# Optimization experiments

Hardware: AMD Instinct MI355X
Metric: run time of the kernel (lower is better)

The kernel has to match this reference:

```python
import jax, jax.numpy as jnp
import numpy as np

N_NODES = 100000
N_EDGES = 3200000
F_IN = 512
HIDDEN = 16
N_CLASSES = 64
EPS = 1e-12  # F.normalize eps


def agnn_layer(x, src, dst, beta, n_nodes):
    """AGNNConv: cosine-similarity attention + segment softmax + scatter aggregate.
    x: [N, H]; src/dst: [E] (messages flow src -> dst, softmax over edges per dst).
    """
    norm = jnp.sqrt(jnp.sum(x * x, axis=-1, keepdims=True))
    xn = x / jnp.maximum(norm, EPS)                      # L2-normalized features
    cos = jnp.sum(xn[src] * xn[dst], axis=-1)            # [E] cosine similarity
    logits = beta * cos
    m = jax.ops.segment_max(logits, dst, num_segments=n_nodes)   # stable softmax per dst
    e = jnp.exp(logits - m[dst])
    denom = jax.ops.segment_sum(e, dst, num_segments=n_nodes)
    alpha = e / denom[dst]                               # [E]
    return jax.ops.segment_sum(alpha[:, None] * x[src], dst, num_segments=n_nodes)


def setup_inputs() -> dict:
    key = jax.random.key(0)
    ks = jax.random.split(key, 6)
    x = jax.random.normal(ks[0], (N_NODES, F_IN), dtype=jnp.float32)
    edge_index = jax.random.randint(ks[1], (2, N_EDGES), 0, N_NODES, dtype=jnp.int64)
    W1 = jax.random.normal(ks[2], (F_IN, HIDDEN), dtype=jnp.float32) * (1.0 / np.sqrt(F_IN))
    b1 = jnp.zeros((HIDDEN,), dtype=jnp.float32)
    W2 = jax.random.normal(ks[3], (HIDDEN, N_CLASSES), dtype=jnp.float32) * (1.0 / np.sqrt(HIDDEN))
    b2 = jnp.zeros((N_CLASSES,), dtype=jnp.float32)
    beta1 = jnp.ones((), dtype=jnp.float32)  # AGNNConv beta init = 1.0
    beta2 = jnp.ones((), dtype=jnp.float32)
    return {"x": x, "edge_index": edge_index, "W1": W1, "b1": b1,
            "W2": W2, "b2": b2, "beta1": beta1, "beta2": beta2}


def reference(x, edge_index, W1, b1, W2, b2, beta1, beta2):
    n = x.shape[0]
    # PyG AGNNConv adds self-loops before propagation
    loops = jnp.arange(n, dtype=edge_index.dtype)
    src = jnp.concatenate([edge_index[0], loops])
    dst = jnp.concatenate([edge_index[1], loops])
    # eval mode: dropout is identity
    h = jax.nn.relu(x @ W1 + b1)                 # [N, 16]
    h = agnn_layer(h, src, dst, beta1, n)
    h = agnn_layer(h, src, dst, beta2, n)
    out = h @ W2 + b2                            # [N, num_classes]
    return jax.nn.log_softmax(out, axis=1)
```

## Files before the change

### kernel.cpp

```cpp
#include <hip/hip_runtime.h>
#include <hip/hip_bf16.h>

#define F_IN 512
#define HID 16
#define NCLS 64
#define NBUCK_MAX 512
#define EPB 8192

__device__ __forceinline__ void gemm_rows(
    const float* __restrict__ x, const float* __restrict__ W1,
    const float* __restrict__ b1, float* __restrict__ h0,
    float* __restrict__ inv0, int rB, int rE, int wid, int totalWaves, int lane)
{
    float bias = b1[lane & 15];
    const bool s3 = (lane & 8) != 0;
    const bool s2 = (lane & 4) != 0;
    const bool s1 = (lane & 2) != 0;
    const bool s0 = (lane & 1) != 0;

    for (int g = rB + wid * 4; g < rE; g += totalWaves * 4) {
        int r0 = g;
        int r1 = (g + 1 < rE) ? g + 1 : rE - 1;
        int r2 = (g + 2 < rE) ? g + 2 : rE - 1;
        int r3 = (g + 3 < rE) ? g + 3 : rE - 1;

        float xv[4][8];
        {
            const float4* xp0 = (const float4*)(x + (size_t)r0 * F_IN + 8 * lane);
            const float4* xp1 = (const float4*)(x + (size_t)r1 * F_IN + 8 * lane);
            const float4* xp2 = (const float4*)(x + (size_t)r2 * F_IN + 8 * lane);
            const float4* xp3 = (const float4*)(x + (size_t)r3 * F_IN + 8 * lane);
            float4 a, b;
            a = xp0[0]; b = xp0[1];
            xv[0][0]=a.x; xv[0][1]=a.y; xv[0][2]=a.z; xv[0][3]=a.w;
            xv[0][4]=b.x; xv[0][5]=b.y; xv[0][6]=b.z; xv[0][7]=b.w;
            a = xp1[0]; b = xp1[1];
            xv[1][0]=a.x; xv[1][1]=a.y; xv[1][2]=a.z; xv[1][3]=a.w;
            xv[1][4]=b.x; xv[1][5]=b.y; xv[1][6]=b.z; xv[1][7]=b.w;
            a = xp2[0]; b = xp2[1];
            xv[2][0]=a.x; xv[2][1]=a.y; xv[2][2]=a.z; xv[2][3]=a.w;
            xv[2][4]=b.x; xv[2][5]=b.y; xv[2][6]=b.z; xv[2][7]=b.w;
            a = xp3[0]; b = xp3[1];
            xv[3][0]=a.x; xv[3][1]=a.y; xv[3][2]=a.z; xv[3][3]=a.w;
            xv[3][4]=b.x; xv[3][5]=b.y; xv[3][6]=b.z; xv[3][7]=b.w;
        }

        float acc[4][16];
#pragma unroll
        for (int i = 0; i < 4; ++i)
#pragma unroll
            for (int j = 0; j < 16; ++j) acc[i][j] = 0.f;

#pragma unroll
        for (int kk = 0; kk < 8; ++kk) {
            const float4* wp = (const float4*)(W1 + (size_t)(8 * lane + kk) * HID);
#pragma unroll
            for (int jj = 0; jj < 4; ++jj) {
                float4 t = wp[jj];
#pragma unroll
                for (int i = 0; i < 4; ++i) {
                    float xs = xv[i][kk];
                    acc[i][jj * 4 + 0] += xs * t.x;
                    acc[i][jj * 4 + 1] += xs * t.y;
                    acc[i][jj * 4 + 2] += xs * t.z;
                    acc[i][jj * 4 + 3] += xs * t.w;
                }
            }
        }

        int rr[4] = {r0, r1, r2, r3};
#pragma unroll
        for (int i = 0; i < 4; ++i) {
            float* a = acc[i];
#pragma unroll
            for (int u = 0; u < 8; ++u) {
                float k = s3 ? a[u + 8] : a[u];
                float s = s3 ? a[u] : a[u + 8];
                a[u] = k + __shfl_xor(s, 8);
            }
#pragma unroll
            for (int u = 0; u < 4; ++u) {
                float k = s2 ? a[u + 4] : a[u];
                float s = s2 ? a[u] : a[u + 4];
                a[u] = k + __shfl_xor(s, 4);
            }
#pragma unroll
            for (int u = 0; u < 2; ++u) {
                float k = s1 ? a[u + 2] : a[u];
                float s = s1 ? a[u] : a[u + 2];
                a[u] = k + __shfl_xor(s, 2);
            }
            {
                float k = s0 ? a[1] : a[0];
                float s = s0 ? a[0] : a[1];
                a[0] = k + __shfl_xor(s, 1);
            }
            a[0] += __shfl_xor(a[0], 16);
            a[0] += __shfl_xor(a[0], 32);

            float val = fmaxf(a[0] + bias, 0.f);
            bool live = (g + i < rE);
            if (live && lane < 16) h0[(size_t)rr[i] * HID + lane] = val;

            float qq = val * val;
            qq += __shfl_xor(qq, 1);
            qq += __shfl_xor(qq, 2);
            qq += __shfl_xor(qq, 4);
            qq += __shfl_xor(qq, 8);
            if (live && lane == 0) inv0[rr[i]] = 1.f / fmaxf(sqrtf(qq), 1e-12f);
        }
    }
}

__global__ __launch_bounds__(256) void hist1_kernel(
    const int* __restrict__ dst, int E, int EV, int nbuck,
    int* __restrict__ bucketCount)
{
    __shared__ int h[NBUCK_MAX];
    int tid = threadIdx.x;
    for (int j = tid; j < nbuck; j += 256) h[j] = 0;
    __syncthreads();
    int base = blockIdx.x * EPB;
    for (int k = 0; k < EPB / 256; ++k) {
        int i = base + k * 256 + tid;
        if (i < EV) {
            int d = (i < E) ? dst[i] : (i - E);
            atomicAdd(&h[d >> 8], 1);
        }
    }
    __syncthreads();
    for (int j = tid; j < nbuck; j += 256)
        if (h[j]) atomicAdd(&bucketCount[j], h[j]);
}

__global__ __launch_bounds__(512) void bucket_scan_kernel(
    const int* __restrict__ bucketCount, int nbuck,
    int* __restrict__ bucketStart, int* __restrict__ gCursor)
{
    __shared__ int s[512];
    int t = threadIdx.x;
    int v = (t < nbuck) ? bucketCount[t] : 0;
    s[t] = v;
    __syncthreads();
    for (int off = 1; off < 512; off <<= 1) {
        int add = (t >= off) ? s[t - off] : 0;
        __syncthreads();
        s[t] += add;
        __syncthreads();
    }
    int incl = s[t];
    if (t < nbuck) {
        bucketStart[t] = incl - v;
        gCursor[t]     = incl - v;
        if (t == nbuck - 1) bucketStart[nbuck] = incl;
    }
}

__global__ __launch_bounds__(256) void part_gemm_kernel(
    const int* __restrict__ src, const int* __restrict__ dst,
    int E, int EV, int nbuck, int* __restrict__ gCursor,
    unsigned* __restrict__ staged,
    const float* __restrict__ x, const float* __restrict__ W1,
    const float* __restrict__ b1, float* __restrict__ h0,
    float* __restrict__ inv0, int rB, int rE, int csrBlocks, int gemmWaves)
{
    __shared__ int h[NBUCK_MAX];
    __shared__ int gb[NBUCK_MAX];
    int tid = threadIdx.x;

    if ((int)blockIdx.x >= csrBlocks) {
        int wid = (((int)blockIdx.x - csrBlocks) * 256 + tid) >> 6;
        gemm_rows(x, W1, b1, h0, inv0, rB, rE, wid, gemmWaves, tid & 63);
        return;
    }

    for (int j = tid; j < nbuck; j += 256) h[j] = 0;
    __syncthreads();

    int base = blockIdx.x * EPB;
    for (int k = 0; k < EPB / 256; ++k) {
        int i = base + k * 256 + tid;
        if (i < EV) {
            int d = (i < E) ? dst[i] : (i - E);
            atomicAdd(&h[d >> 8], 1);
        }
    }
    __syncthreads();
    for (int j = tid; j < nbuck; j += 256) {
        int c = h[j];
        if (c) gb[j] = atomicAdd(&gCursor[j], c);
        h[j] = 0;
    }
    __syncthreads();
    for (int k = 0; k < EPB / 256; ++k) {
        int i = base + k * 256 + tid;
        if (i < EV) {
            int s, d;
            if (i < E) { s = src[i]; d = dst[i]; }
            else       { s = i - E;  d = s; }
            int bkt = d >> 8;
            int ofs = atomicAdd(&h[bkt], 1);
            staged[gb[bkt] + ofs] = (unsigned)s | ((unsigned)(d & 255) << 17);
        }
    }
}

__global__ __launch_bounds__(256) void build_gemm_kernel(
    const unsigned* __restrict__ staged, const int* __restrict__ bucketStart,
    int* __restrict__ counts, int* __restrict__ rowstart,
    int* __restrict__ esrc, int N,
    const float* __restrict__ x, const float* __restrict__ W1,
    const float* __restrict__ b1, float* __restrict__ h0,
    float* __restrict__ inv0, int rB, int rE, int csrBlocks, int gemmWaves)
{
    __shared__ int hist[256];
    __shared__ int s[256];
    __shared__ int cur[256];
    int tid = threadIdx.x;

    if ((int)blockIdx.x >= csrBlocks) {
        int wid = (((int)blockIdx.x - csrBlocks) * 256 + tid) >> 6;
        gemm_rows(x, W1, b1, h0, inv0, rB, rE, wid, gemmWaves, tid & 63);
        return;
    }

    int b   = blockIdx.x;
    int start = bucketStart[b];
    int end   = bucketStart[b + 1];

    hist[tid] = 0;
    __syncthreads();
    for (int i = start + tid; i < end; i += 256)
        atomicAdd(&hist[(staged[i] >> 17) & 255], 1);
    __syncthreads();

    int v = hist[tid];
    s[tid] = v;
    __syncthreads();
    for (int off = 1; off < 256; off <<= 1) {
        int add = (tid >= off) ? s[tid - off] : 0;
        __syncthreads();
        s[tid] += add;
        __syncthreads();
    }
    int excl = s[tid] - v;
    int dstg = b * 256 + tid;
    if (dstg < N) {
        counts[dstg]   = v;
        rowstart[dstg] = start + excl;
    }
    cur[tid] = start + excl;
    __syncthreads();

    for (int i = start + tid; i < end; i += 256) {
        unsigned pk = staged[i];
        int dl  = (pk >> 17) & 255;
        int pos = atomicAdd(&cur[dl], 1);
        esrc[pos] = (int)(pk & 0x1FFFFu);
    }
}

__global__ __launch_bounds__(256) void agg_kernel(
    const float* __restrict__ h, const float* __restrict__ inv,
    const int* __restrict__ esrc, const int* __restrict__ rowstart,
    const int* __restrict__ counts, const float* __restrict__ beta_p,
    float* __restrict__ hout, float* __restrict__ invout, int N)
{
    int node = (blockIdx.x * blockDim.x + threadIdx.x) >> 6;
    if (node >= N) return;
    int lane = threadIdx.x & 63;
    int q = lane & 3;
    int e = lane >> 2;

    float beta  = *beta_p;
    float shift = fabsf(beta);
    float4 hd4  = ((const float4*)(h + (size_t)node * HID))[q];
    float  invd = inv[node];
    int start = rowstart[node];
    int cnt   = counts[node];

    int t0 = e, t1 = e + 16, t2 = e + 32, t3 = e + 48;
    int s0 = esrc[start + (t0 < cnt ? t0 : 0)];
    int s1 = esrc[start + (t1 < cnt ? t1 : 0)];
    int s2 = esrc[start + (t2 < cnt ? t2 : 0)];
    int s3 = esrc[start + (t3 < cnt ? t3 : 0)];
    const float4* hp = (const float4*)h;
    float4 a0 = hp[(size_t)s0 * 4 + q];
    float4 a1 = hp[(size_t)s1 * 4 + q];
    float4 a2 = hp[(size_t)s2 * 4 + q];
    float4 a3 = hp[(size_t)s3 * 4 + q];
    float i0 = inv[s0], i1 = inv[s1], i2 = inv[s2], i3 = inv[s3];

    float denom = 0.f;
    float4 acc = make_float4(0.f, 0.f, 0.f, 0.f);

#define AGG_SLOT(aa, ii, tt)                                                  \
    {                                                                         \
        float p = aa.x * hd4.x + aa.y * hd4.y + aa.z * hd4.z + aa.w * hd4.w;  \
        p += __shfl_xor(p, 1);                                                \
        p += __shfl_xor(p, 2);                                                \
        float w = __expf(beta * (p * invd * ii) - shift);                     \
        w = (tt < cnt) ? w : 0.f;                                             \
        denom += w;                                                           \
        acc.x += w * aa.x; acc.y += w * aa.y;                                 \
        acc.z += w * aa.z; acc.w += w * aa.w;                                 \
    }
    AGG_SLOT(a0, i0, t0)
    AGG_SLOT(a1, i1, t1)
    AGG_SLOT(a2, i2, t2)
    AGG_SLOT(a3, i3, t3)
#undef AGG_SLOT

    for (int t = e + 64; t < cnt; t += 16) {
        int sr = esrc[start + t];
        float4 hs4 = hp[(size_t)sr * 4 + q];
        float invs = inv[sr];
        float p = hs4.x * hd4.x + hs4.y * hd4.y + hs4.z * hd4.z + hs4.w * hd4.w;
        p += __shfl_xor(p, 1);
        p += __shfl_xor(p, 2);
        float w = __expf(beta * (p * invd * invs) - shift);
        denom += w;
        acc.x += w * hs4.x;
        acc.y += w * hs4.y;
        acc.z += w * hs4.z;
        acc.w += w * hs4.w;
    }

#pragma unroll
    for (int off = 4; off <= 32; off <<= 1) {
        denom += __shfl_xor(denom, off);
        acc.x += __shfl_xor(acc.x, off);
        acc.y += __shfl_xor(acc.y, off);
        acc.z += __shfl_xor(acc.z, off);
        acc.w += __shfl_xor(acc.w, off);
    }
    float rd = 1.f / denom;
    float4 o = make_float4(acc.x * rd, acc.y * rd, acc.z * rd, acc.w * rd);
    if (lane < 4) ((float4*)(hout + (size_t)node * HID))[q] = o;

    float ss = o.x * o.x + o.y * o.y + o.z * o.z + o.w * o.w;
    ss += __shfl_xor(ss, 1);
    ss += __shfl_xor(ss, 2);
    if (lane == 0) invout[node] = 1.f / fmaxf(sqrtf(ss), 1e-12f);
}

__global__ __launch_bounds__(256) void out_kernel(
    const float* __restrict__ h2, const float* __restrict__ W2,
    const float* __restrict__ b2, float* __restrict__ out, int N)
{
    int wave = (blockIdx.x * blockDim.x + threadIdx.x) >> 6;
    int lane = threadIdx.x & 63;
    if (wave >= N) return;

    float hv = (lane < HID) ? h2[(size_t)wave * HID + lane] : 0.f;
    float acc = b2[lane];
#pragma unroll
    for (int k = 0; k < HID; ++k) {
        float hk = __shfl(hv, k);
        acc += hk * W2[k * NCLS + lane];
    }
    float m = acc;
    for (int off = 32; off > 0; off >>= 1) m = fmaxf(m, __shfl_xor(m, off));
    float e = __expf(acc - m);
    float ssum = e;
    for (int off = 32; off > 0; off >>= 1) ssum += __shfl_xor(ssum, off);
    out[(size_t)wave * NCLS + lane] = (acc - m) - __logf(ssum);
}

extern "C" void kernel_launch(void* const* d_in, const int* in_sizes, int n_in,
                              void* d_out, int out_size, void* d_ws, size_t ws_size,
                              hipStream_t stream)
{
    const float* x     = (const float*)d_in[0];
    const int*   eidx  = (const int*)d_in[1];
    const float* W1    = (const float*)d_in[2];
    const float* b1    = (const float*)d_in[3];
    const float* W2    = (const float*)d_in[4];
    const float* b2    = (const float*)d_in[5];
    const float* beta1 = (const float*)d_in[6];
    const float* beta2 = (const float*)d_in[7];

    int N = in_sizes[0] / F_IN;
    int E = in_sizes[1] / 2;
    const int* src = eidx;
    const int* dst = eidx + E;
    float* out = (float*)d_out;

    int EV    = E + N;
    int nbuck = (N + 255) / 256;

    char* wptr = (char*)d_ws;
    auto alloc = [&](size_t bytes) -> char* {
        char* p = wptr;
        wptr += (bytes + 255) / 256 * 256;
        return p;
    };
    float*    h0       = (float*)alloc((size_t)N * HID * 4);
    float*    inv0     = (float*)alloc((size_t)N * 4);
    float*    h1       = (float*)alloc((size_t)N * HID * 4);
    float*    inv1     = (float*)alloc((size_t)N * 4);
    float*    h2       = (float*)alloc((size_t)N * HID * 4);
    float*    inv2     = (float*)alloc((size_t)N * 4);
    int*      counts   = (int*)alloc((size_t)N * 4);
    int*      rowstart = (int*)alloc((size_t)(N + 1) * 4);
    int*      esrc     = (int*)alloc((size_t)EV * 4);
    unsigned* staged   = (unsigned*)alloc((size_t)EV * 4);
    int*      bucketCount = (int*)alloc((size_t)(nbuck + 1) * 4);
    int*      bucketStart = (int*)alloc((size_t)(nbuck + 1) * 4);
    int*      gCursor     = (int*)alloc((size_t)nbuck * 4);

    int ebBlocks = (EV + EPB - 1) / EPB;

    hipMemsetAsync(bucketCount, 0, (size_t)nbuck * 4, stream);
    hist1_kernel<<<ebBlocks, 256, 0, stream>>>(dst, E, EV, nbuck, bucketCount);
    bucket_scan_kernel<<<1, 512, 0, stream>>>(bucketCount, nbuck, bucketStart, gCursor);

    int rSplit   = 60000;
    int gcBlocks = 1024;
    int gdBlocks = 768;
    part_gemm_kernel<<<ebBlocks + gcBlocks, 256, 0, stream>>>(
        src, dst, E, EV, nbuck, gCursor, staged,
        x, W1, b1, h0, inv0, 0, rSplit, ebBlocks, gcBlocks * 4);
    build_gemm_kernel<<<nbuck + gdBlocks, 256, 0, stream>>>(
        staged, bucketStart, counts, rowstart, esrc, N,
        x, W1, b1, h0, inv0, rSplit, N, nbuck, gdBlocks * 4);

    int aggBlocks = (N + 3) / 4;
    agg_kernel<<<aggBlocks, 256, 0, stream>>>(h0, inv0, esrc, rowstart, counts, beta1,
                                              h1, inv1, N);
    agg_kernel<<<aggBlocks, 256, 0, stream>>>(h1, inv1, esrc, rowstart, counts, beta2,
                                              h2, inv2, N);

    out_kernel<<<(N * 64 + 255) / 256, 256, 0, stream>>>(h2, W2, b2, out, N);
}
```

Before: 552.5 us.

## Fuse partition, CSR build, GEMM, aggregations and output into one cooperative kernel

Replaces five separate launches (partition+GEMM, build+GEMM, two aggregation passes, output) with one persistent cooperative mega-kernel that uses grid.sync between phases. The partition and CSR build run on a quarter of the resident blocks while the rest compute the input GEMM. The GEMM inner loop drops from 4 rows to 2 rows per wave to cut register pressure for the occupancy hint. The aim is to remove launch gaps and kernel tails. The cost is grid-wide barriers, a grid capped by occupancy with grid-stride loops, and a fixed 55/45 GEMM split that may not balance the two phases.

```diff
diff --git a/kernel.cpp b/kernel.cpp
--- a/kernel.cpp
+++ b/kernel.cpp
@@ -1,5 +1,7 @@
 #include <hip/hip_runtime.h>
-#include <hip/hip_bf16.h>
+#include <hip/hip_cooperative_groups.h>
+
+namespace cg = cooperative_groups;
 
 #define F_IN 512
 #define HID 16
@@ -7,7 +9,7 @@
 #define NBUCK_MAX 512
 #define EPB 8192
 
-__device__ __forceinline__ void gemm_rows(
+__device__ __forceinline__ void gemm_rows2(
     const float* __restrict__ x, const float* __restrict__ W1,
     const float* __restrict__ b1, float* __restrict__ h0,
     float* __restrict__ inv0, int rB, int rE, int wid, int totalWaves, int lane)
@@ -18,18 +20,14 @@
     const bool s1 = (lane & 2) != 0;
     const bool s0 = (lane & 1) != 0;
 
-    for (int g = rB + wid * 4; g < rE; g += totalWaves * 4) {
+    for (int g = rB + wid * 2; g < rE; g += totalWaves * 2) {
         int r0 = g;
         int r1 = (g + 1 < rE) ? g + 1 : rE - 1;
-        int r2 = (g + 2 < rE) ? g + 2 : rE - 1;
-        int r3 = (g + 3 < rE) ? g + 3 : rE - 1;
-
-        float xv[4][8];
+
+        float xv[2][8];
         {
             const float4* xp0 = (const float4*)(x + (size_t)r0 * F_IN + 8 * lane);
             const float4* xp1 = (const float4*)(x + (size_t)r1 * F_IN + 8 * lane);
-            const float4* xp2 = (const float4*)(x + (size_t)r2 * F_IN + 8 * lane);
-            const float4* xp3 = (const float4*)(x + (size_t)r3 * F_IN + 8 * lane);
             float4 a, b;
             a = xp0[0]; b = xp0[1];
             xv[0][0]=a.x; xv[0][1]=a.y; xv[0][2]=a.z; xv[0][3]=a.w;
@@ -37,17 +35,11 @@
             a = xp1[0]; b = xp1[1];
             xv[1][0]=a.x; xv[1][1]=a.y; xv[1][2]=a.z; xv[1][3]=a.w;
             xv[1][4]=b.x; xv[1][5]=b.y; xv[1][6]=b.z; xv[1][7]=b.w;
-            a = xp2[0]; b = xp2[1];
-            xv[2][0]=a.x; xv[2][1]=a.y; xv[2][2]=a.z; xv[2][3]=a.w;
-            xv[2][4]=b.x; xv[2][5]=b.y; xv[2][6]=b.z; xv[2][7]=b.w;
-            a = xp3[0]; b = xp3[1];
-            xv[3][0]=a.x; xv[3][1]=a.y; xv[3][2]=a.z; xv[3][3]=a.w;
-            xv[3][4]=b.x; xv[3][5]=b.y; xv[3][6]=b.z; xv[3][7]=b.w;
-        }
-
-        float acc[4][16];
-#pragma unroll
-        for (int i = 0; i < 4; ++i)
+        }
+
+        float acc[2][16];
+#pragma unroll
+        for (int i = 0; i < 2; ++i)
 #pragma unroll
             for (int j = 0; j < 16; ++j) acc[i][j] = 0.f;
 
@@ -58,7 +50,7 @@
             for (int jj = 0; jj < 4; ++jj) {
                 float4 t = wp[jj];
 #pragma unroll
-                for (int i = 0; i < 4; ++i) {
+                for (int i = 0; i < 2; ++i) {
                     float xs = xv[i][kk];
                     acc[i][jj * 4 + 0] += xs * t.x;
                     acc[i][jj * 4 + 1] += xs * t.y;
@@ -68,9 +60,9 @@
             }
         }
 
-        int rr[4] = {r0, r1, r2, r3};
-#pragma unroll
-        for (int i = 0; i < 4; ++i) {
+        int rr[2] = {r0, r1};
+#pragma unroll
+        for (int i = 0; i < 2; ++i) {
             float* a = acc[i];
 #pragma unroll
             for (int u = 0; u < 8; ++u) {
@@ -109,6 +101,118 @@
             qq += __shfl_xor(qq, 8);
             if (live && lane == 0) inv0[rr[i]] = 1.f / fmaxf(sqrtf(qq), 1e-12f);
         }
+    }
+}
+
+__device__ __forceinline__ void agg_phase(
+    const float* __restrict__ h, const float* __restrict__ inv,
+    const int* __restrict__ esrc, const int* __restrict__ rowstart,
+    const int* __restrict__ counts, const float* __restrict__ beta_p,
+    float* __restrict__ hout, float* __restrict__ invout, int N, int G)
+{
+    int w = blockIdx.x * 4 + (threadIdx.x >> 6);
+    int W = G * 4;
+    int lane = threadIdx.x & 63;
+    int q = lane & 3;
+    int e = lane >> 2;
+
+    float beta  = *beta_p;
+    float shift = fabsf(beta);
+    const float4* hp = (const float4*)h;
+
+    for (int node = w; node < N; node += W) {
+        float4 hd4  = hp[(size_t)node * 4 + q];
+        float  invd = inv[node];
+        int start = rowstart[node];
+        int cnt   = counts[node];
+
+        int t0 = e, t1 = e + 16, t2 = e + 32, t3 = e + 48;
+        int s0 = esrc[start + (t0 < cnt ? t0 : 0)];
+        int s1 = esrc[start + (t1 < cnt ? t1 : 0)];
+        int s2 = esrc[start + (t2 < cnt ? t2 : 0)];
+        int s3 = esrc[start + (t3 < cnt ? t3 : 0)];
+        float4 a0 = hp[(size_t)s0 * 4 + q];
+        float4 a1 = hp[(size_t)s1 * 4 + q];
+        float4 a2 = hp[(size_t)s2 * 4 + q];
+        float4 a3 = hp[(size_t)s3 * 4 + q];
+        float i0 = inv[s0], i1 = inv[s1], i2 = inv[s2], i3 = inv[s3];
+
+        float denom = 0.f;
+        float4 acc = make_float4(0.f, 0.f, 0.f, 0.f);
+
+#define AGG_SLOT(aa, ii, tt)                                                  \
+        {                                                                     \
+            float p = aa.x*hd4.x + aa.y*hd4.y + aa.z*hd4.z + aa.w*hd4.w;      \
+            p += __shfl_xor(p, 1);                                            \
+            p += __shfl_xor(p, 2);                                            \
+            float wgt = __expf(beta * (p * invd * ii) - shift);               \
+            wgt = (tt < cnt) ? wgt : 0.f;                                     \
+            denom += wgt;                                                     \
+            acc.x += wgt * aa.x; acc.y += wgt * aa.y;                         \
+            acc.z += wgt * aa.z; acc.w += wgt * aa.w;                         \
+        }
+        AGG_SLOT(a0, i0, t0)
+        AGG_SLOT(a1, i1, t1)
+        AGG_SLOT(a2, i2, t2)
+        AGG_SLOT(a3, i3, t3)
+#undef AGG_SLOT
+
+        for (int t = e + 64; t < cnt; t += 16) {
+            int sr = esrc[start + t];
+            float4 hs4 = hp[(size_t)sr * 4 + q];
+            float invs = inv[sr];
+            float p = hs4.x*hd4.x + hs4.y*hd4.y + hs4.z*hd4.z + hs4.w*hd4.w;
+            p += __shfl_xor(p, 1);
+            p += __shfl_xor(p, 2);
+            float wgt = __expf(beta * (p * invd * invs) - shift);
+            denom += wgt;
+            acc.x += wgt * hs4.x;
+            acc.y += wgt * hs4.y;
+            acc.z += wgt * hs4.z;
+            acc.w += wgt * hs4.w;
+        }
+
+#pragma unroll
+        for (int off = 4; off <= 32; off <<= 1) {
+            denom += __shfl_xor(denom, off);
+            acc.x += __shfl_xor(acc.x, off);
+            acc.y += __shfl_xor(acc.y, off);
+            acc.z += __shfl_xor(acc.z, off);
+            acc.w += __shfl_xor(acc.w, off);
+        }
+        float rd = 1.f / denom;
+        float4 o = make_float4(acc.x * rd, acc.y * rd, acc.z * rd, acc.w * rd);
+        if (lane < 4) ((float4*)(hout + (size_t)node * HID))[q] = o;
+
+        float ss = o.x*o.x + o.y*o.y + o.z*o.z + o.w*o.w;
+        ss += __shfl_xor(ss, 1);
+        ss += __shfl_xor(ss, 2);
+        if (lane == 0) invout[node] = 1.f / fmaxf(sqrtf(ss), 1e-12f);
+    }
+}
+
+__device__ __forceinline__ void out_phase(
+    const float* __restrict__ h2, const float* __restrict__ W2,
+    const float* __restrict__ b2, float* __restrict__ out, int N, int G)
+{
+    int w = blockIdx.x * 4 + (threadIdx.x >> 6);
+    int W = G * 4;
+    int lane = threadIdx.x & 63;
+
+    for (int row = w; row < N; row += W) {
+        float hv = (lane < HID) ? h2[(size_t)row * HID + lane] : 0.f;
+        float acc = b2[lane];
+#pragma unroll
+        for (int k = 0; k < HID; ++k) {
+            float hk = __shfl(hv, k);
+            acc += hk * W2[k * NCLS + lane];
+        }
+        float m = acc;
+        for (int off = 32; off > 0; off >>= 1) m = fmaxf(m, __shfl_xor(m, off));
+        float e = __expf(acc - m);
+        float ssum = e;
+        for (int off = 32; off > 0; off >>= 1) ssum += __shfl_xor(ssum, off);
+        out[(size_t)row * NCLS + lane] = (acc - m) - __logf(ssum);
     }
 }
 
@@ -156,215 +260,114 @@
     }
 }
 
-__global__ __launch_bounds__(256) void part_gemm_kernel(
-    const int* __restrict__ src, const int* __restrict__ dst,
-    int E, int EV, int nbuck, int* __restrict__ gCursor,
-    unsigned* __restrict__ staged,
-    const float* __restrict__ x, const float* __restrict__ W1,
-    const float* __restrict__ b1, float* __restrict__ h0,
-    float* __restrict__ inv0, int rB, int rE, int csrBlocks, int gemmWaves)
-{
-    __shared__ int h[NBUCK_MAX];
-    __shared__ int gb[NBUCK_MAX];
+struct MegaArgs {
+    const int* src; const int* dst; int E; int EV; int nbuck;
+    int* gCursor; unsigned* staged;
+    const int* bucketStart; int* counts; int* rowstart; int* esrc; int N;
+    const float* x; const float* W1; const float* b1;
+    float* h0; float* inv0; float* h1; float* inv1; float* h2; float* inv2;
+    const float* beta1; const float* beta2;
+    const float* W2; const float* b2; float* out;
+    int C; int G; int splitA;
+};
+
+__global__ __launch_bounds__(256, 6) void mega_kernel(MegaArgs a)
+{
+    cg::grid_group grid = cg::this_grid();
+    __shared__ int lh[NBUCK_MAX];
+    __shared__ int lg[NBUCK_MAX];
+    int bid = blockIdx.x;
     int tid = threadIdx.x;
-
-    if ((int)blockIdx.x >= csrBlocks) {
-        int wid = (((int)blockIdx.x - csrBlocks) * 256 + tid) >> 6;
-        gemm_rows(x, W1, b1, h0, inv0, rB, rE, wid, gemmWaves, tid & 63);
-        return;
-    }
-
-    for (int j = tid; j < nbuck; j += 256) h[j] = 0;
-    __syncthreads();
-
-    int base = blockIdx.x * EPB;
-    for (int k = 0; k < EPB / 256; ++k) {
-        int i = base + k * 256 + tid;
-        if (i < EV) {
-            int d = (i < E) ? dst[i] : (i - E);
-            atomicAdd(&h[d >> 8], 1);
-        }
-    }
-    __syncthreads();
-    for (int j = tid; j < nbuck; j += 256) {
-        int c = h[j];
-        if (c) gb[j] = atomicAdd(&gCursor[j], c);
-        h[j] = 0;
-    }
-    __syncthreads();
-    for (int k = 0; k < EPB / 256; ++k) {
-        int i = base + k * 256 + tid;
-        if (i < EV) {
+    int lane = tid & 63;
+
+    if (bid < a.C) {
+        int chunk = (a.EV + a.C - 1) / a.C;
+        int base = bid * chunk;
+        int lim  = base + chunk; if (lim > a.EV) lim = a.EV;
+
+        for (int j = tid; j < a.nbuck; j += 256) lh[j] = 0;
+        __syncthreads();
+        for (int i = base + tid; i < lim; i += 256) {
+            int d = (i < a.E) ? a.dst[i] : (i - a.E);
+            atomicAdd(&lh[d >> 8], 1);
+        }
+        __syncthreads();
+        for (int j = tid; j < a.nbuck; j += 256) {
+            int c = lh[j];
+            if (c) lg[j] = atomicAdd(&a.gCursor[j], c);
+            lh[j] = 0;
+        }
+        __syncthreads();
+        for (int i = base + tid; i < lim; i += 256) {
             int s, d;
-            if (i < E) { s = src[i]; d = dst[i]; }
-            else       { s = i - E;  d = s; }
+            if (i < a.E) { s = a.src[i]; d = a.dst[i]; }
+            else         { s = i - a.E;  d = s; }
             int bkt = d >> 8;
-            int ofs = atomicAdd(&h[bkt], 1);
-            staged[gb[bkt] + ofs] = (unsigned)s | ((unsigned)(d & 255) << 17);
-        }
-    }
-}
-
-__global__ __launch_bounds__(256) void build_gemm_kernel(
-    const unsigned* __restrict__ staged, const int* __restrict__ bucketStart,
-    int* __restrict__ counts, int* __restrict__ rowstart,
-    int* __restrict__ esrc, int N,
-    const float* __restrict__ x, const float* __restrict__ W1,
-    const float* __restrict__ b1, float* __restrict__ h0,
-    float* __restrict__ inv0, int rB, int rE, int csrBlocks, int gemmWaves)
-{
-    __shared__ int hist[256];
-    __shared__ int s[256];
-    __shared__ int cur[256];
-    int tid = threadIdx.x;
-
-    if ((int)blockIdx.x >= csrBlocks) {
-        int wid = (((int)blockIdx.x - csrBlocks) * 256 + tid) >> 6;
-        gemm_rows(x, W1, b1, h0, inv0, rB, rE, wid, gemmWaves, tid & 63);
-        return;
-    }
-
-    int b   = blockIdx.x;
-    int start = bucketStart[b];
-    int end   = bucketStart[b + 1];
-
-    hist[tid] = 0;
-    __syncthreads();
-    for (int i = start + tid; i < end; i += 256)
-        atomicAdd(&hist[(staged[i] >> 17) & 255], 1);
-    __syncthreads();
-
-    int v = hist[tid];
-    s[tid] = v;
-    __syncthreads();
-    for (int off = 1; off < 256; off <<= 1) {
-        int add = (tid >= off) ? s[tid - off] : 0;
-        __syncthreads();
-        s[tid] += add;
-        __syncthreads();
-    }
-    int excl = s[tid] - v;
-    int dstg = b * 256 + tid;
-    if (dstg < N) {
-        counts[dstg]   = v;
-        rowstart[dstg] = start + excl;
-    }
-    cur[tid] = start + excl;
-    __syncthreads();
-
-    for (int i = start + tid; i < end; i += 256) {
-        unsigned pk = staged[i];
-        int dl  = (pk >> 17) & 255;
-        int pos = atomicAdd(&cur[dl], 1);
-        esrc[pos] = (int)(pk & 0x1FFFFu);
-    }
-}
-
-__global__ __launch_bounds__(256) void agg_kernel(
-    const float* __restrict__ h, const float* __restrict__ inv,
-    const int* __restrict__ esrc, const int* __restrict__ rowstart,
-    const int* __restrict__ counts, const float* __restrict__ beta_p,
-    float* __restrict__ hout, float* __restrict__ invout, int N)
-{
-    int node = (blockIdx.x * blockDim.x + threadIdx.x) >> 6;
-    if (node >= N) return;
-    int lane = threadIdx.x & 63;
-    int q = lane & 3;
-    int e = lane >> 2;
-
-    float beta  = *beta_p;
-    float shift = fabsf(beta);
-    float4 hd4  = ((const float4*)(h + (size_t)node * HID))[q];
-    float  invd = inv[node];
-    int start = rowstart[node];
-    int cnt   = counts[node];
-
-    int t0 = e, t1 = e + 16, t2 = e + 32, t3 = e + 48;
-    int s0 = esrc[start + (t0 < cnt ? t0 : 0)];
-    int s1 = esrc[start + (t1 < cnt ? t1 : 0)];
-    int s2 = esrc[start + (t2 < cnt ? t2 : 0)];
-    int s3 = esrc[start + (t3 < cnt ? t3 : 0)];
-    const float4* hp = (const float4*)h;
-    float4 a0 = hp[(size_t)s0 * 4 + q];
-    float4 a1 = hp[(size_t)s1 * 4 + q];
-    float4 a2 = hp[(size_t)s2 * 4 + q];
-    float4 a3 = hp[(size_t)s3 * 4 + q];
-    float i0 = inv[s0], i1 = inv[s1], i2 = inv[s2], i3 = inv[s3];
-
-    float denom = 0.f;
-    float4 acc = make_float4(0.f, 0.f, 0.f, 0.f);
-
-#define AGG_SLOT(aa, ii, tt)                                                  \
-    {                                                                         \
-        float p = aa.x * hd4.x + aa.y * hd4.y + aa.z * hd4.z + aa.w * hd4.w;  \
-        p += __shfl_xor(p, 1);                                                \
-        p += __shfl_xor(p, 2);                                                \
-        float w = __expf(beta * (p * invd * ii) - shift);                     \
-        w = (tt < cnt) ? w : 0.f;                                             \
-        denom += w;                                                           \
-        acc.x += w * aa.x; acc.y += w * aa.y;                                 \
-        acc.z += w * aa.z; acc.w += w * aa.w;                                 \
-    }
-    AGG_SLOT(a0, i0, t0)
-    AGG_SLOT(a1, i1, t1)
-    AGG_SLOT(a2, i2, t2)
-    AGG_SLOT(a3, i3, t3)
-#undef AGG_SLOT
-
-    for (int t = e + 64; t < cnt; t += 16) {
-        int sr = esrc[start + t];
-        float4 hs4 = hp[(size_t)sr * 4 + q];
-        float invs = inv[sr];
-        float p = hs4.x * hd4.x + hs4.y * hd4.y + hs4.z * hd4.z + hs4.w * hd4.w;
-        p += __shfl_xor(p, 1);
-        p += __shfl_xor(p, 2);
-        float w = __expf(beta * (p * invd * invs) - shift);
-        denom += w;
-        acc.x += w * hs4.x;
-        acc.y += w * hs4.y;
-        acc.z += w * hs4.z;
-        acc.w += w * hs4.w;
-    }
-
-#pragma unroll
-    for (int off = 4; off <= 32; off <<= 1) {
-        denom += __shfl_xor(denom, off);
-        acc.x += __shfl_xor(acc.x, off);
-        acc.y += __shfl_xor(acc.y, off);
-        acc.z += __shfl_xor(acc.z, off);
-        acc.w += __shfl_xor(acc.w, off);
-    }
-    float rd = 1.f / denom;
-    float4 o = make_float4(acc.x * rd, acc.y * rd, acc.z * rd, acc.w * rd);
-    if (lane < 4) ((float4*)(hout + (size_t)node * HID))[q] = o;
-
-    float ss = o.x * o.x + o.y * o.y + o.z * o.z + o.w * o.w;
-    ss += __shfl_xor(ss, 1);
-    ss += __shfl_xor(ss, 2);
-    if (lane == 0) invout[node] = 1.f / fmaxf(sqrtf(ss), 1e-12f);
-}
-
-__global__ __launch_bounds__(256) void out_kernel(
-    const float* __restrict__ h2, const float* __restrict__ W2,
-    const float* __restrict__ b2, float* __restrict__ out, int N)
-{
-    int wave = (blockIdx.x * blockDim.x + threadIdx.x) >> 6;
-    int lane = threadIdx.x & 63;
-    if (wave >= N) return;
-
-    float hv = (lane < HID) ? h2[(size_t)wave * HID + lane] : 0.f;
-    float acc = b2[lane];
-#pragma unroll
-    for (int k = 0; k < HID; ++k) {
-        float hk = __shfl(hv, k);
-        acc += hk * W2[k * NCLS + lane];
-    }
-    float m = acc;
-    for (int off = 32; off > 0; off >>= 1) m = fmaxf(m, __shfl_xor(m, off));
-    float e = __expf(acc - m);
-    float ssum = e;
-    for (int off = 32; off > 0; off >>= 1) ssum += __shfl_xor(ssum, off);
-    out[(size_t)wave * NCLS + lane] = (acc - m) - __logf(ssum);
+            int ofs = atomicAdd(&lh[bkt], 1);
+            a.staged[lg[bkt] + ofs] = (unsigned)s | ((unsigned)(d & 255) << 17);
+        }
+    } else {
+        int wid = (bid - a.C) * 4 + (tid >> 6);
+        gemm_rows2(a.x, a.W1, a.b1, a.h0, a.inv0, 0, a.splitA,
+                   wid, (a.G - a.C) * 4, lane);
+    }
+    grid.sync();
+
+    if (bid < a.C) {
+        int* hist = lh;
+        int* sArr = lh + 256;
+        int* cur  = lg;
+        for (int b = bid; b < a.nbuck; b += a.C) {
+            int start = a.bucketStart[b];
+            int end   = a.bucketStart[b + 1];
+
+            hist[tid] = 0;
+            __syncthreads();
+            for (int i = start + tid; i < end; i += 256)
+                atomicAdd(&hist[(a.staged[i] >> 17) & 255], 1);
+            __syncthreads();
+
+            int v = hist[tid];
+            sArr[tid] = v;
+            __syncthreads();
+            for (int off = 1; off < 256; off <<= 1) {
+                int add = (tid >= off) ? sArr[tid - off] : 0;
+                __syncthreads();
+                sArr[tid] += add;
+                __syncthreads();
+            }
+            int excl = sArr[tid] - v;
+            int dstg = b * 256 + tid;
+            if (dstg < a.N) {
+                a.counts[dstg]   = v;
+                a.rowstart[dstg] = start + excl;
+            }
+            cur[tid] = start + excl;
+            __syncthreads();
+
+            for (int i = start + tid; i < end; i += 256) {
+                unsigned pk = a.staged[i];
+                int dl  = (pk >> 17) & 255;
+                int pos = atomicAdd(&cur[dl], 1);
+                a.esrc[pos] = (int)(pk & 0x1FFFFu);
+            }
+            __syncthreads();
+        }
+    } else {
+        int wid = (bid - a.C) * 4 + (tid >> 6);
+        gemm_rows2(a.x, a.W1, a.b1, a.h0, a.inv0, a.splitA, a.N,
+                   wid, (a.G - a.C) * 4, lane);
+    }
+    grid.sync();
+
+    agg_phase(a.h0, a.inv0, a.esrc, a.rowstart, a.counts, a.beta1,
+              a.h1, a.inv1, a.N, a.G);
+    grid.sync();
+    agg_phase(a.h1, a.inv1, a.esrc, a.rowstart, a.counts, a.beta2,
+              a.h2, a.inv2, a.N, a.G);
+    grid.sync();
+
+    out_phase(a.h2, a.W2, a.b2, a.out, a.N, a.G);
 }
 
 extern "C" void kernel_launch(void* const* d_in, const int* in_sizes, int n_in,
@@ -411,25 +414,38 @@
 
     int ebBlocks = (EV + EPB - 1) / EPB;
 
+    static int gBlocks = 0;
+    if (gBlocks == 0) {
+        hipDeviceProp_t prop;
+        hipGetDeviceProperties(&prop, 0);
+        int perCU = 0;
+        hipOccupancyMaxActiveBlocksPerMultiprocessor(&perCU, mega_kernel, 256, 0);
+        if (perCU < 1) perCU = 1;
+        long long g = (long long)perCU * prop.multiProcessorCount;
+        gBlocks = (g > 1536) ? 1536 : (int)g;
+    }
+    int G = gBlocks;
+    int C = G / 4;
+    if (C < 1) C = 1;
+    int splitA = (int)((long long)N * 55 / 100);
+
     hipMemsetAsync(bucketCount, 0, (size_t)nbuck * 4, stream);
     hist1_kernel<<<ebBlocks, 256, 0, stream>>>(dst, E, EV, nbuck, bucketCount);
     bucket_scan_kernel<<<1, 512, 0, stream>>>(bucketCount, nbuck, bucketStart, gCursor);
 
-    int rSplit   = 60000;
-    int gcBlocks = 1024;
-    int gdBlocks = 768;
-    part_gemm_kernel<<<ebBlocks + gcBlocks, 256, 0, stream>>>(
-        src, dst, E, EV, nbuck, gCursor, staged,
-        x, W1, b1, h0, inv0, 0, rSplit, ebBlocks, gcBlocks * 4);
-    build_gemm_kernel<<<nbuck + gdBlocks, 256, 0, stream>>>(
-        staged, bucketStart, counts, rowstart, esrc, N,
-        x, W1, b1, h0, inv0, rSplit, N, nbuck, gdBlocks * 4);
-
-    int aggBlocks = (N + 3) / 4;
-    agg_kernel<<<aggBlocks, 256, 0, stream>>>(h0, inv0, esrc, rowstart, counts, beta1,
-                                              h1, inv1, N);
-    agg_kernel<<<aggBlocks, 256, 0, stream>>>(h1, inv1, esrc, rowstart, counts, beta2,
-                                              h2, inv2, N);
-
-    out_kernel<<<(N * 64 + 255) / 256, 256, 0, stream>>>(h2, W2, b2, out, N);
-}
+    MegaArgs ma;
+    ma.src = src; ma.dst = dst; ma.E = E; ma.EV = EV; ma.nbuck = nbuck;
+    ma.gCursor = gCursor; ma.staged = staged;
+    ma.bucketStart = bucketStart; ma.counts = counts; ma.rowstart = rowstart;
+    ma.esrc = esrc; ma.N = N;
+    ma.x = x; ma.W1 = W1; ma.b1 = b1;
+    ma.h0 = h0; ma.inv0 = inv0; ma.h1 = h1; ma.inv1 = inv1;
+    ma.h2 = h2; ma.inv2 = inv2;
+    ma.beta1 = beta1; ma.beta2 = beta2;
+    ma.W2 = W2; ma.b2 = b2; ma.out = out;
+    ma.C = C; ma.G = G; ma.splitA = splitA;
+
+    void* kargs[] = { (void*)&ma };
+    hipLaunchCooperativeKernel(reinterpret_cast<void*>(mega_kernel),
+                               dim3(G), dim3(256), kargs, 0, stream);
+}
```

New measurement: 1.364 ms. 147% more time.

## Fuse bucket scan into histogram kernel and output head into last aggregation

Applied to the files above, without the earlier changes.

The histogram kernel now counts finished blocks with a global atomic, and the last block to finish runs the 512-entry bucket prefix scan, which removes the separate single-block scan launch. The second aggregation layer is templated so its final variant computes the 16x64 output projection and log-softmax in-register, which removes the h2/inv2 round trip and the separate output kernel. This saves two kernel launches and some memory traffic. In exchange the last histogram block runs the scan serially, and the fused output epilogue adds register pressure to the aggregation kernel.

```diff
diff --git a/kernel.cpp b/kernel.cpp
--- a/kernel.cpp
+++ b/kernel.cpp
@@ -112,11 +112,14 @@
     }
 }
 
-__global__ __launch_bounds__(256) void hist1_kernel(
-    const int* __restrict__ dst, int E, int EV, int nbuck,
-    int* __restrict__ bucketCount)
+__global__ __launch_bounds__(256) void histscan_kernel(
+    const int* __restrict__ dst, int E, int EV, int nbuck, int nblocks,
+    int* __restrict__ bucketCount, int* __restrict__ doneCnt,
+    int* __restrict__ bucketStart, int* __restrict__ gCursor)
 {
     __shared__ int h[NBUCK_MAX];
+    __shared__ int s[NBUCK_MAX];
+    __shared__ int lastFlag;
     int tid = threadIdx.x;
     for (int j = tid; j < nbuck; j += 256) h[j] = 0;
     __syncthreads();
@@ -131,29 +134,35 @@
     __syncthreads();
     for (int j = tid; j < nbuck; j += 256)
         if (h[j]) atomicAdd(&bucketCount[j], h[j]);
-}
-
-__global__ __launch_bounds__(512) void bucket_scan_kernel(
-    const int* __restrict__ bucketCount, int nbuck,
-    int* __restrict__ bucketStart, int* __restrict__ gCursor)
-{
-    __shared__ int s[512];
-    int t = threadIdx.x;
-    int v = (t < nbuck) ? bucketCount[t] : 0;
-    s[t] = v;
+
+    __threadfence();
+    __syncthreads();
+    if (tid == 0) {
+        int prev = atomicAdd(doneCnt, 1);
+        lastFlag = (prev == nblocks - 1) ? 1 : 0;
+    }
+    __syncthreads();
+    if (!lastFlag) return;
+
+    int i1 = tid + 256;
+    int v0 = (tid < nbuck) ? atomicAdd(&bucketCount[tid], 0) : 0;
+    int v1 = (i1  < nbuck) ? atomicAdd(&bucketCount[i1],  0) : 0;
+    s[tid] = v0;
+    s[i1]  = v1;
     __syncthreads();
     for (int off = 1; off < 512; off <<= 1) {
-        int add = (t >= off) ? s[t - off] : 0;
+        int a0 = (tid >= off) ? s[tid - off] : 0;
+        int a1 = (i1  >= off) ? s[i1  - off] : 0;
         __syncthreads();
-        s[t] += add;
+        s[tid] += a0;
+        s[i1]  += a1;
         __syncthreads();
     }
-    int incl = s[t];
-    if (t < nbuck) {
-        bucketStart[t] = incl - v;
-        gCursor[t]     = incl - v;
-        if (t == nbuck - 1) bucketStart[nbuck] = incl;
-    }
+    int incl0 = s[tid], incl1 = s[i1];
+    if (tid < nbuck) { bucketStart[tid] = incl0 - v0; gCursor[tid] = incl0 - v0; }
+    if (i1  < nbuck) { bucketStart[i1]  = incl1 - v1; gCursor[i1]  = incl1 - v1; }
+    if (tid == nbuck - 1) bucketStart[nbuck] = incl0;
+    if (i1  == nbuck - 1) bucketStart[nbuck] = incl1;
 }
 
 __global__ __launch_bounds__(256) void part_gemm_kernel(
@@ -260,11 +269,14 @@
     }
 }
 
+template<int LAST>
 __global__ __launch_bounds__(256) void agg_kernel(
     const float* __restrict__ h, const float* __restrict__ inv,
     const int* __restrict__ esrc, const int* __restrict__ rowstart,
     const int* __restrict__ counts, const float* __restrict__ beta_p,
-    float* __restrict__ hout, float* __restrict__ invout, int N)
+    float* __restrict__ hout, float* __restrict__ invout,
+    const float* __restrict__ W2, const float* __restrict__ b2,
+    float* __restrict__ out, int N)
 {
     int node = (blockIdx.x * blockDim.x + threadIdx.x) >> 6;
     if (node >= N) return;
@@ -336,35 +348,34 @@
     }
     float rd = 1.f / denom;
     float4 o = make_float4(acc.x * rd, acc.y * rd, acc.z * rd, acc.w * rd);
-    if (lane < 4) ((float4*)(hout + (size_t)node * HID))[q] = o;
-
-    float ss = o.x * o.x + o.y * o.y + o.z * o.z + o.w * o.w;
-    ss += __shfl_xor(ss, 1);
-    ss += __shfl_xor(ss, 2);
-    if (lane == 0) invout[node] = 1.f / fmaxf(sqrtf(ss), 1e-12f);
-}
-
-__global__ __launch_bounds__(256) void out_kernel(
-    const float* __restrict__ h2, const float* __restrict__ W2,
-    const float* __restrict__ b2, float* __restrict__ out, int N)
-{
-    int wave = (blockIdx.x * blockDim.x + threadIdx.x) >> 6;
-    int lane = threadIdx.x & 63;
-    if (wave >= N) return;
-
-    float hv = (lane < HID) ? h2[(size_t)wave * HID + lane] : 0.f;
-    float acc = b2[lane];
-#pragma unroll
-    for (int k = 0; k < HID; ++k) {
-        float hk = __shfl(hv, k);
-        acc += hk * W2[k * NCLS + lane];
-    }
-    float m = acc;
-    for (int off = 32; off > 0; off >>= 1) m = fmaxf(m, __shfl_xor(m, off));
-    float e = __expf(acc - m);
-    float ssum = e;
-    for (int off = 32; off > 0; off >>= 1) ssum += __shfl_xor(ssum, off);
-    out[(size_t)wave * NCLS + lane] = (acc - m) - __logf(ssum);
+
+    if (!LAST) {
+        if (lane < 4) ((float4*)(hout + (size_t)node * HID))[q] = o;
+        float ss = o.x * o.x + o.y * o.y + o.z * o.z + o.w * o.w;
+        ss += __shfl_xor(ss, 1);
+        ss += __shfl_xor(ss, 2);
+        if (lane == 0) invout[node] = 1.f / fmaxf(sqrtf(ss), 1e-12f);
+    } else {
+        float h2f[16];
+#pragma unroll
+        for (int qp = 0; qp < 4; ++qp) {
+            int srcl = (lane & ~3) | qp;
+            h2f[4 * qp + 0] = __shfl(o.x, srcl);
+            h2f[4 * qp + 1] = __shfl(o.y, srcl);
+            h2f[4 * qp + 2] = __shfl(o.z, srcl);
+            h2f[4 * qp + 3] = __shfl(o.w, srcl);
+        }
+        float logit = b2[lane];
+#pragma unroll
+        for (int k = 0; k < HID; ++k)
+            logit += h2f[k] * W2[k * NCLS + lane];
+        float m = logit;
+        for (int off = 32; off > 0; off >>= 1) m = fmaxf(m, __shfl_xor(m, off));
+        float ex = __expf(logit - m);
+        float ssum = ex;
+        for (int off = 32; off > 0; off >>= 1) ssum += __shfl_xor(ssum, off);
+        out[(size_t)node * NCLS + lane] = (logit - m) - __logf(ssum);
+    }
 }
 
 extern "C" void kernel_launch(void* const* d_in, const int* in_sizes, int n_in,
@@ -399,21 +410,21 @@
     float*    inv0     = (float*)alloc((size_t)N * 4);
     float*    h1       = (float*)alloc((size_t)N * HID * 4);
     float*    inv1     = (float*)alloc((size_t)N * 4);
-    float*    h2       = (float*)alloc((size_t)N * HID * 4);
-    float*    inv2     = (float*)alloc((size_t)N * 4);
     int*      counts   = (int*)alloc((size_t)N * 4);
     int*      rowstart = (int*)alloc((size_t)(N + 1) * 4);
     int*      esrc     = (int*)alloc((size_t)EV * 4);
     unsigned* staged   = (unsigned*)alloc((size_t)EV * 4);
-    int*      bucketCount = (int*)alloc((size_t)(nbuck + 1) * 4);
+    int*      bucketCount = (int*)alloc((size_t)(nbuck + 2) * 4);
     int*      bucketStart = (int*)alloc((size_t)(nbuck + 1) * 4);
     int*      gCursor     = (int*)alloc((size_t)nbuck * 4);
+    int*      doneCnt     = bucketCount + nbuck + 1;
 
     int ebBlocks = (EV + EPB - 1) / EPB;
 
-    hipMemsetAsync(bucketCount, 0, (size_t)nbuck * 4, stream);
-    hist1_kernel<<<ebBlocks, 256, 0, stream>>>(dst, E, EV, nbuck, bucketCount);
-    bucket_scan_kernel<<<1, 512, 0, stream>>>(bucketCount, nbuck, bucketStart, gCursor);
+    hipMemsetAsync(bucketCount, 0, (size_t)(nbuck + 2) * 4, stream);
+    histscan_kernel<<<ebBlocks, 256, 0, stream>>>(dst, E, EV, nbuck, ebBlocks,
+                                                  bucketCount, doneCnt,
+                                                  bucketStart, gCursor);
 
     int rSplit   = 60000;
     int gcBlocks = 1024;
@@ -426,10 +437,13 @@
         x, W1, b1, h0, inv0, rSplit, N, nbuck, gdBlocks * 4);
 
     int aggBlocks = (N + 3) / 4;
-    agg_kernel<<<aggBlocks, 256, 0, stream>>>(h0, inv0, esrc, rowstart, counts, beta1,
-                                              h1, inv1, N);
-    agg_kernel<<<aggBlocks, 256, 0, stream>>>(h1, inv1, esrc, rowstart, counts, beta2,
-                                              h2, inv2, N);
-
-    out_kernel<<<(N * 64 + 255) / 256, 256, 0, stream>>>(h2, W2, b2, out, N);
-}
+    agg_kernel<0><<<aggBlocks, 256, 0, stream>>>(h0, inv0, esrc, rowstart, counts,
+                                                 beta1, h1, inv1,
+                                                 (const float*)nullptr,
+                                                 (const float*)nullptr,
+                                                 (float*)nullptr, N);
+    agg_kernel<1><<<aggBlocks, 256, 0, stream>>>(h1, inv1, esrc, rowstart, counts,
+                                                 beta2, (float*)nullptr,
+                                                 (float*)nullptr,
+                                                 W2, b2, out, N);
+}
```

Result: no change. 559.2 us (+1.2%).
